# Kernel optimization log

Measured on AMD Instinct MI355X. Metric: run time of the kernel, lower is better.

Reference implementation:

```python
import jax, jax.numpy as jnp
import numpy as np

# C2fBoT config (matches init_kwargs)
B, C1, C2, N, F, HEADS, E = 8, 512, 512, 2, 32, 4, 0.5
C = int(C2 * E)          # hidden channels = 256
HD = C // HEADS          # head_dim = 64
BN_EPS = 1e-3            # ultralytics Conv uses BatchNorm2d(eps=0.001)


def conv2d(x, w, pad):
    # x: [B,Cin,H,W], w: [Cout,Cin,kh,kw]
    return jax.lax.conv_general_dilated(
        x, w, (1, 1), [(pad, pad), (pad, pad)],
        dimension_numbers=("NCHW", "OIHW", "NCHW"))


def bn_eval(x, p):
    # p: [4,C] rows = gamma, beta, running_mean, running_var (inference BN)
    g, b, m, v = p
    s = (g / jnp.sqrt(v + BN_EPS))[:, None, None]
    return (x - m[:, None, None]) * s + b[:, None, None]


def cbs(x, w, p, pad):
    # YOLO Conv block: Conv2d -> BN -> SiLU
    return jax.nn.silu(bn_eval(conv2d(x, w, pad), p))


def bot_attention(x, qkv_w, rw, rh):
    # x: [B,C,H,W]; 1x1-conv QKV + learned relative position bias
    b, c, h, w = x.shape
    hw = h * w
    qkv = conv2d(x, qkv_w, 0).reshape(b, 3, HEADS, HD, hw)
    q, k, v = qkv[:, 0], qkv[:, 1], qkv[:, 2]           # [B,heads,hd,HW]
    r = (rw + rh).reshape(1, HEADS, HD, hw)              # rel-pos content
    # q^T@k*scale + q^T@r*scale == q^T@(k+r)*scale (r broadcasts over batch)
    logits = jnp.einsum('bhdi,bhdj->bhij', q, k + r) * (HD ** -0.5)
    a = jax.nn.softmax(logits, axis=-1)                  # [B,heads,HW,HW]
    out = jnp.einsum('bhij,bhdj->bhdi', a, v)            # [B,heads,hd,HW]
    return out.reshape(b, c, h, w)


def setup_inputs() -> dict:
    key = jax.random.key(0)
    ks = iter(jax.random.split(key, 32))
    def nrm(shape, s=0.05):
        return jax.random.normal(next(ks), shape, jnp.float32) * s
    def bnp(cc):
        return jnp.stack([
            1.0 + 0.1 * jax.random.normal(next(ks), (cc,), jnp.float32),  # gamma
            0.1 * jax.random.normal(next(ks), (cc,), jnp.float32),        # beta
            0.1 * jax.random.normal(next(ks), (cc,), jnp.float32),        # mean
            0.5 + jax.random.uniform(next(ks), (cc,), jnp.float32),       # var
        ])
    return {
        "x": jax.random.normal(next(ks), (B, C1, F, F), jnp.float32),
        "cv1_w": nrm((2 * C, C1, 1, 1)),
        "cv1_bn": bnp(2 * C),
        "cv2_w": nrm((C2, (2 + N) * C, 1, 1)),
        "cv2_bn": bnp(C2),
        "m_cv1_w": nrm((N, C, C, 3, 3)),
        "m_cv1_bn": jnp.stack([bnp(C) for _ in range(N)]),
        "m_qkv_w": nrm((N, 3 * C, C, 1, 1)),
        "m_rw": jax.random.normal(next(ks), (N, 1, HEADS, HD, 1, F), jnp.float32),
        "m_rh": jax.random.normal(next(ks), (N, 1, HEADS, HD, F, 1), jnp.float32),
        "m_cv2_w": nrm((N, C, C, 1, 1)),
        "m_cv2_bn": jnp.stack([bnp(C) for _ in range(N)]),
    }


def reference(x, cv1_w, cv1_bn, cv2_w, cv2_bn,
              m_cv1_w, m_cv1_bn, m_qkv_w, m_rw, m_rh, m_cv2_w, m_cv2_bn):
    t = cbs(x, cv1_w, cv1_bn, 0)                 # [B,2C,H,W]
    ys = [t[:, :C], t[:, C:]]                    # chunk(2, dim=1)
    for i in range(N):                           # fixed small layer loop
        yi = ys[-1]
        z = cbs(yi, m_cv1_w[i], m_cv1_bn[i], 1)  # 3x3 Conv-BN-SiLU
        z = bot_attention(z, m_qkv_w[i], m_rw[i], m_rh[i])
        z = jax.nn.silu(bn_eval(conv2d(z, m_cv2_w[i], 0), m_cv2_bn[i]))
        ys.append(yi + z)                        # shortcut (c1 == c2)
    return cbs(jnp.concatenate(ys, axis=1), cv2_w, cv2_bn, 0)
```

## Files before the change

kernel.cpp:

```cpp
#include <hip/hip_runtime.h>
#include <hip/hip_bf16.h>

typedef unsigned short ushort_t;
typedef __bf16 bf16x8 __attribute__((ext_vector_type(8)));
typedef float f32x4 __attribute__((ext_vector_type(4)));
typedef unsigned short us8 __attribute__((ext_vector_type(8)));
typedef unsigned short us4 __attribute__((ext_vector_type(4)));

#define AS1 __attribute__((address_space(1)))
#define AS3 __attribute__((address_space(3)))

#if __has_builtin(__builtin_amdgcn_exp2f)
#define EXP2F __builtin_amdgcn_exp2f
#else
#define EXP2F exp2f
#endif

__device__ __forceinline__ void gld16(const void* g, void* l){
  __builtin_amdgcn_global_load_lds((AS1 void*)(void*)g, (AS3 void*)l, 16, 0, 0);
}
__device__ __forceinline__ f32x4 mfma16(bf16x8 a, bf16x8 b, f32x4 c){
  return __builtin_amdgcn_mfma_f32_16x16x32_bf16(a, b, c, 0, 0, 0);
}
__device__ __forceinline__ unsigned short f2bfu(float f){
  union { float f; unsigned int i; } c; c.f = f;
  unsigned int x = c.i;
  return (unsigned short)((x + 0x7fffu + ((x >> 16) & 1u)) >> 16);
}
__device__ __forceinline__ float bfu2f(unsigned short u){
  union { unsigned int i; float f; } c; c.i = ((unsigned int)u) << 16; return c.f;
}
__device__ __forceinline__ float dsilu(float x){ return x / (1.f + __expf(-x)); }

__global__ __launch_bounds__(256)
void transpose_x_k(const float* __restrict__ x, ushort_t* __restrict__ xc)
{
  __shared__ float tl[64*68];
  const int ci0 = blockIdx.x*64, px0 = blockIdx.y*64, b = blockIdx.z;
  const int t = threadIdx.x;
  {
    const int ci_l = t>>2, pc = (t&3)*16;
    const float* src = x + (size_t)b*524288 + (size_t)(ci0+ci_l)*1024 + px0 + pc;
    float* d = &tl[ci_l*68 + pc];
    *(float4*)(d)    = *(const float4*)(src);
    *(float4*)(d+4)  = *(const float4*)(src+4);
    *(float4*)(d+8)  = *(const float4*)(src+8);
    *(float4*)(d+12) = *(const float4*)(src+12);
  }
  __syncthreads();
  {
    const int px_l = t>>2, cc = (t&3)*16;
    us8 o0, o1;
#pragma unroll
    for (int i = 0; i < 8; i++) o0[i] = f2bfu(tl[(cc+i)*68 + px_l]);
#pragma unroll
    for (int i = 0; i < 8; i++) o1[i] = f2bfu(tl[(cc+8+i)*68 + px_l]);
    ushort_t* dst = xc + (size_t)b*524288 + (size_t)(px0+px_l)*512 + ci0 + cc;
    *(us8*)dst = o0; *(us8*)(dst+8) = o1;
  }
}

__global__ __launch_bounds__(256)
void cvt4_k(const float* s0, const float* s1, const float* s2, const float* s3,
            ushort_t* d0, ushort_t* d1, ushort_t* d2, ushort_t* d3,
            int n0, int n1, int n2, int n3)
{
  const int seg = blockIdx.y;
  const float* s = (seg==0?s0:seg==1?s1:seg==2?s2:s3);
  ushort_t* d    = (seg==0?d0:seg==1?d1:seg==2?d2:d3);
  const int n4   = (seg==0?n0:seg==1?n1:seg==2?n2:n3) >> 2;
  for (int i = blockIdx.x*256 + threadIdx.x; i < n4; i += gridDim.x*256){
    const float4 v = *(const float4*)(s + (size_t)i*4);
    ushort4 p; p.x=f2bfu(v.x); p.y=f2bfu(v.y); p.z=f2bfu(v.z); p.w=f2bfu(v.w);
    *(ushort4*)(d + (size_t)i*4) = p;
  }
}

__global__ __launch_bounds__(256)
void reorder3_k(const float* __restrict__ w, ushort_t* __restrict__ o,
                ushort_t* __restrict__ zb)
{
  const int blk = blockIdx.x;
  if (blk == 0 && threadIdx.x < 64) zb[threadIdx.x] = 0;
  const float* src = w + (size_t)blk*2304;
  ushort_t* dst = o + (size_t)blk*2304;
  for (int idx = threadIdx.x; idx < 2304; idx += 256){
    const int ci = idx/9, tap = idx - ci*9;
    dst[tap*256 + ci] = f2bfu(src[idx]);
  }
}

template<int BMODE, int EPI, int NT>
__global__ __launch_bounds__(256, 4)
void gemm_k(const ushort_t* __restrict__ A, const int M, const int K, const int kplen,
            const ushort_t* __restrict__ B0, const ushort_t* __restrict__ B1,
            const ushort_t* __restrict__ B2, const ushort_t* __restrict__ B3,
            const int Rb, const long Bbs,
            const float* __restrict__ bnp,
            const float* __restrict__ rw, const float* __restrict__ rh,
            const ushort_t* __restrict__ res, const long res_bs, const int res_rs,
            ushort_t* __restrict__ vtout, const ushort_t* __restrict__ zb,
            void* __restrict__ outp, const long out_bs, const int out_rs)
{
  constexpr int NW = NT/4;
  constexpr int NF = NW/16;
  constexpr int CH = 8 + NT/8;
  constexpr int CPW = CH/4;
  const int m0 = blockIdx.x*64, n0 = blockIdx.y*NT;
  const int bz = blockIdx.z, b = bz & 7, part = bz >> 3;
  const int tid = threadIdx.x, lane = tid & 63, w = tid >> 6;
  const int q = lane >> 4, l15 = lane & 15;
  const int crow8 = lane >> 3, kq8 = lane & 7;
  const int gq8 = kq8 ^ crow8;
  const int r7 = l15 & 7;
  __shared__ __align__(16) ushort_t A_s[64*64];
  __shared__ __align__(16) ushort_t B_s[NT*64];

  f32x4 acc[4][NF];
#pragma unroll
  for (int mi = 0; mi < 4; mi++)
#pragma unroll
    for (int ni = 0; ni < NF; ni++) acc[mi][ni] = (f32x4){0.f,0.f,0.f,0.f};

  const int kbeg = part*kplen, kend_ = kbeg + kplen;
  for (int k0 = kbeg; k0 < kend_; k0 += 64){
    const int kk = k0 + gq8*8;
#pragma unroll
    for (int p = 0; p < CPW; p++){
      const int c = w*CPW + p;
      if (c < 8){
        const int row = c*8 + crow8;
        gld16(A + (size_t)(m0 + row)*K + kk, A_s + c*512);
      } else {
        const int cb = c - 8;
        const int row = cb*8 + crow8;
        const ushort_t* gb;
        if (BMODE == 0){
          gb = B0 + (size_t)b*Bbs + (size_t)(n0 + row)*Rb + kk;
        } else if (BMODE == 1){
          const int seg = kk >> 8;
          const ushort_t* sb = (seg==0?B0:seg==1?B1:seg==2?B2:B3);
          const int sstr = (seg < 2) ? 512 : 256;
          const long sbs = (seg < 2) ? 524288L : 262144L;
          gb = sb + (size_t)b*sbs + (size_t)(n0 + row)*sstr + (kk & 255);
        } else {
          const int tap = k0 >> 8;
          const int ci = (k0 & 255) + gq8*8;
          const int oy = tap/3 - 1, ox = tap - (tap/3)*3 - 1;
          const int px = n0 + row;
          const int yy = (px >> 5) + oy, xx = (px & 31) + ox;
          const bool vld = ((unsigned)yy < 32u) && ((unsigned)xx < 32u);
          gb = vld ? (B0 + (size_t)b*Bbs + (size_t)(yy*32 + xx)*Rb + ci) : zb;
        }
        gld16(gb, B_s + cb*512);
      }
    }
    __syncthreads();
#pragma unroll
    for (int ks = 0; ks < 2; ks++){
      const int slot = (ks*4 + q) ^ r7;
      bf16x8 af[4], bfr[NF];
#pragma unroll
      for (int mi = 0; mi < 4; mi++)
        af[mi] = __builtin_bit_cast(bf16x8, *(const us8*)&A_s[(mi*16 + l15)*64 + slot*8]);
#pragma unroll
      for (int ni = 0; ni < NF; ni++)
        bfr[ni] = __builtin_bit_cast(bf16x8, *(const us8*)&B_s[(w*NW + ni*16 + l15)*64 + slot*8]);
#pragma unroll
      for (int mi = 0; mi < 4; mi++)
#pragma unroll
        for (int ni = 0; ni < NF; ni++)
          acc[mi][ni] = mfma16(af[mi], bfr[ni], acc[mi][ni]);
    }
    __syncthreads();
  }

  const int n_w = n0 + w*NW;
#pragma unroll
  for (int mi = 0; mi < 4; mi++){
    const int mb = m0 + mi*16 + q*4;
    float sc[4], off[4];
    if (EPI != 1 && EPI != 4){
      const float4 g  = *(const float4*)(bnp + mb);
      const float4 be = *(const float4*)(bnp + M + mb);
      const float4 mu = *(const float4*)(bnp + 2*M + mb);
      const float4 va = *(const float4*)(bnp + 3*M + mb);
      sc[0] = g.x/sqrtf(va.x+1e-3f); off[0] = be.x - mu.x*sc[0];
      sc[1] = g.y/sqrtf(va.y+1e-3f); off[1] = be.y - mu.y*sc[1];
      sc[2] = g.z/sqrtf(va.z+1e-3f); off[2] = be.z - mu.z*sc[2];
      sc[3] = g.w/sqrtf(va.w+1e-3f); off[3] = be.w - mu.w*sc[3];
    }
    const int region = mb >> 8;
#pragma unroll
    for (int ni = 0; ni < NF; ni++){
      const int n_g = n_w + ni*16 + l15;
      f32x4 v = acc[mi][ni];
      if (EPI == 4){
        *(float4*)((float*)outp + ((size_t)(part*8 + b)*1024 + n_g)*256 + mb) =
            (float4){v[0], v[1], v[2], v[3]};
        continue;
      }
      float o[4];
#pragma unroll
      for (int r = 0; r < 4; r++){
        float xv = v[r];
        if (EPI == 1){
          if (region == 0) xv *= 0.18033688011112042f;
          else if (region == 1){
            const int c64 = mb + r - 256;
            xv += rw[c64*32 + (n_g & 31)] + rh[c64*32 + (n_g >> 5)];
          }
        } else {
          xv = dsilu(xv*sc[r] + off[r]);
          if (EPI == 2)
            xv += bfu2f(res[(size_t)b*res_bs + (size_t)n_g*res_rs + mb + r]);
        }
        o[r] = xv;
      }
      if (EPI == 3){
        float* of = (float*)outp + (size_t)b*out_bs;
#pragma unroll
        for (int r = 0; r < 4; r++) of[(size_t)(mb + r)*1024 + n_g] = o[r];
      } else if (EPI == 1 && region == 2){
#pragma unroll
        for (int r = 0; r < 4; r++)
          vtout[(size_t)b*262144 + (size_t)(mb + r - 512)*1024 + n_g] = f2bfu(o[r]);
      } else {
        ushort4 pk; pk.x=f2bfu(o[0]); pk.y=f2bfu(o[1]); pk.z=f2bfu(o[2]); pk.w=f2bfu(o[3]);
        *(ushort4*)((ushort_t*)outp + (size_t)b*out_bs + (size_t)n_g*out_rs + mb) = pk;
      }
    }
  }
}

__global__ __launch_bounds__(256)
void reduce3_k(const float* __restrict__ pbuf, const float* __restrict__ bnp,
               ushort_t* __restrict__ out)
{
  const int idx = blockIdx.x*256 + threadIdx.x;
  const int co = (idx & 63)*4;
  const size_t e = (size_t)idx*4;
  float4 a = *(const float4*)(pbuf + e);
  const float4 c = *(const float4*)(pbuf + 2097152 + e);
  a.x += c.x; a.y += c.y; a.z += c.z; a.w += c.w;
  const float4 g  = *(const float4*)(bnp + co);
  const float4 be = *(const float4*)(bnp + 256 + co);
  const float4 mu = *(const float4*)(bnp + 512 + co);
  const float4 va = *(const float4*)(bnp + 768 + co);
  float s0 = g.x/sqrtf(va.x+1e-3f), s1 = g.y/sqrtf(va.y+1e-3f);
  float s2 = g.z/sqrtf(va.z+1e-3f), s3 = g.w/sqrtf(va.w+1e-3f);
  ushort4 pk;
  pk.x = f2bfu(dsilu((a.x - mu.x)*s0 + be.x));
  pk.y = f2bfu(dsilu((a.y - mu.y)*s1 + be.y));
  pk.z = f2bfu(dsilu((a.z - mu.z)*s2 + be.z));
  pk.w = f2bfu(dsilu((a.w - mu.w)*s3 + be.w));
  *(ushort4*)(out + e) = pk;
}

__global__ __launch_bounds__(256)
void attn_k(const ushort_t* __restrict__ qk, const ushort_t* __restrict__ vt,
            ushort_t* __restrict__ out)
{
  const int it = blockIdx.x, h = blockIdx.y, b = blockIdx.z;
  const int tid = threadIdx.x, lane = tid & 63, w = tid >> 6;
  const int q = lane >> 4, l15 = lane & 15;
  const int i0 = it*64;
  __shared__ __align__(16) ushort_t K_s[2][4096];
  __shared__ __align__(16) ushort_t V_s[2][4096];
  __shared__ __align__(16) ushort_t P_s[4096];

  const ushort_t* qkb = qk + (size_t)b*524288;
  const ushort_t* vtb = vt + (size_t)b*262144 + (size_t)h*1024*64;

  const int srow = lane >> 3;
  const int sgq  = (lane & 7) ^ srow;
  const int rs7  = l15 & 7;

  bf16x8 qf[2];
  {
    const ushort_t* qr = qkb + (size_t)(i0 + w*16 + l15)*512 + h*64 + q*8;
    qf[0] = __builtin_bit_cast(bf16x8, *(const us8*)qr);
    qf[1] = __builtin_bit_cast(bf16x8, *(const us8*)(qr + 32));
  }
  f32x4 oacc[4];
#pragma unroll
  for (int nd = 0; nd < 4; nd++) oacc[nd] = (f32x4){0.f,0.f,0.f,0.f};
  float m_s = -3e38f, l_s = 0.f;

#define STAGE(JT, BUF) {                                                        \
    const int j0s = (JT)*64;                                                    \
    _Pragma("unroll")                                                           \
    for (int p = 0; p < 2; p++){                                                \
      const int c = w*2 + p;                                                    \
      const int row = c*8 + srow;                                               \
      gld16(qkb + (size_t)(j0s + row)*512 + 256 + h*64 + sgq*8, &K_s[BUF][c*512]); \
      gld16(vtb + (size_t)row*1024 + j0s + sgq*8, &V_s[BUF][c*512]);            \
    }                                                                           \
  }

  STAGE(0, 0);
  int cur = 0;
  for (int jt = 0; jt < 16; jt++){
    __syncthreads();
    if (jt < 15){ STAGE(jt+1, cur^1); }
    f32x4 sacc[4];
#pragma unroll
    for (int ni = 0; ni < 4; ni++) sacc[ni] = (f32x4){0.f,0.f,0.f,0.f};
#pragma unroll
    for (int ks = 0; ks < 2; ks++){
      const int slot = (ks*4 + q) ^ rs7;
#pragma unroll
      for (int ni = 0; ni < 4; ni++){
        const bf16x8 kf = __builtin_bit_cast(bf16x8,
            *(const us8*)&K_s[cur][(ni*16 + l15)*64 + slot*8]);
        sacc[ni] = mfma16(kf, qf[ks], sacc[ni]);
      }
    }
    float mx = sacc[0][0];
#pragma unroll
    for (int ni = 0; ni < 4; ni++)
#pragma unroll
      for (int r = 0; r < 4; r++) mx = fmaxf(mx, sacc[ni][r]);
    mx = fmaxf(mx, __shfl_xor(mx, 16));
    mx = fmaxf(mx, __shfl_xor(mx, 32));
    const float mnew = fmaxf(m_s, mx);
    const float alpha = EXP2F(m_s - mnew);
    m_s = mnew;
    float p[4][4];
    float ps = 0.f;
#pragma unroll
    for (int ni = 0; ni < 4; ni++)
#pragma unroll
      for (int r = 0; r < 4; r++){ p[ni][r] = EXP2F(sacc[ni][r] - mnew); ps += p[ni][r]; }
    ps += __shfl_xor(ps, 16);
    ps += __shfl_xor(ps, 32);
    l_s = l_s*alpha + ps;
#pragma unroll
    for (int r = 0; r < 4; r++){
      const float a_r = __shfl(alpha, q*4 + r);
#pragma unroll
      for (int nd = 0; nd < 4; nd++) oacc[nd][r] *= a_r;
    }
    {
      const int prow = w*16 + l15;
#pragma unroll
      for (int ni = 0; ni < 4; ni++){
        const int qtr = ni*2 + (q>>1);
        us4 pk = { f2bfu(p[ni][0]), f2bfu(p[ni][1]), f2bfu(p[ni][2]), f2bfu(p[ni][3]) };
        *(us4*)&P_s[prow*64 + ((qtr ^ rs7)<<3) + ((q&1)<<2)] = pk;
      }
    }
#pragma unroll
    for (int ks = 0; ks < 2; ks++){
      const int slot = (ks*4 + q) ^ rs7;
      const bf16x8 pa = __builtin_bit_cast(bf16x8,
          *(const us8*)&P_s[(w*16 + l15)*64 + slot*8]);
#pragma unroll
      for (int nd = 0; nd < 4; nd++){
        const bf16x8 vb = __builtin_bit_cast(bf16x8,
            *(const us8*)&V_s[cur][(nd*16 + l15)*64 + slot*8]);
        oacc[nd] = mfma16(pa, vb, oacc[nd]);
      }
    }
    cur ^= 1;
  }
#undef STAGE
  ushort_t* ob = out + (size_t)b*262144;
#pragma unroll
  for (int r = 0; r < 4; r++){
    const float rinv = 1.f / __shfl(l_s, q*4 + r);
    const size_t rowo = (size_t)(i0 + w*16 + q*4 + r)*256 + h*64 + l15;
#pragma unroll
    for (int nd = 0; nd < 4; nd++)
      ob[rowo + nd*16] = f2bfu(oacc[nd][r]*rinv);
  }
}

extern "C" void kernel_launch(void* const* d_in, const int* in_sizes, int n_in,
                              void* d_out, int out_size, void* d_ws, size_t ws_size,
                              hipStream_t stream)
{
  const float* x       = (const float*)d_in[0];
  const float* cv1_w   = (const float*)d_in[1];
  const float* cv1_bn  = (const float*)d_in[2];
  const float* cv2_w   = (const float*)d_in[3];
  const float* cv2_bn  = (const float*)d_in[4];
  const float* mcv1_w  = (const float*)d_in[5];
  const float* mcv1_bn = (const float*)d_in[6];
  const float* mqkv_w  = (const float*)d_in[7];
  const float* mrw     = (const float*)d_in[8];
  const float* mrh     = (const float*)d_in[9];
  const float* mcv2_w  = (const float*)d_in[10];
  const float* mcv2_bn = (const float*)d_in[11];

  ushort_t* uw = (ushort_t*)d_ws;
  ushort_t* x_cl    = uw;
  ushort_t* t_cl    = x_cl    + 4194304;
  ushort_t* wb_cv1  = t_cl    + 4194304;
  ushort_t* wb_cv2  = wb_cv1  + 262144;
  ushort_t* wb_qkv  = wb_cv2  + 524288;
  ushort_t* wb_mcv2 = wb_qkv  + 393216;
  ushort_t* wb_mcv1 = wb_mcv2 + 131072;
  ushort_t* z1_cl   = wb_mcv1 + 1179648;
  ushort_t* qk_cl   = z1_cl   + 2097152;
  ushort_t* vt_b    = qk_cl   + 4194304;
  ushort_t* att_cl  = vt_b    + 2097152;
  ushort_t* y2_cl   = att_cl  + 2097152;
  ushort_t* y3_cl   = y2_cl   + 2097152;
  float*    part_f  = (float*)(y3_cl + 2097152);
  ushort_t* zbuf    = (ushort_t*)(part_f + 4194304);

  const dim3 blk(256);

  transpose_x_k<<<dim3(8,16,8), blk, 0, stream>>>(x, x_cl);
  cvt4_k<<<dim3(256,4), blk, 0, stream>>>(cv1_w, cv2_w, mqkv_w, mcv2_w,
                                          wb_cv1, wb_cv2, wb_qkv, wb_mcv2,
                                          262144, 524288, 393216, 131072);
  reorder3_k<<<dim3(512), blk, 0, stream>>>(mcv1_w, wb_mcv1, zbuf);

  gemm_k<0,0,128><<<dim3(8,8,8), blk, 0, stream>>>(
      wb_cv1, 512, 512, 512, x_cl, nullptr, nullptr, nullptr, 512, 524288L,
      cv1_bn, nullptr, nullptr, nullptr, 0, 0, nullptr, nullptr, t_cl, 524288L, 512);

  const ushort_t* yi = t_cl + 256;  long yi_bs = 524288; int yi_rs = 512;
  ushort_t* youts[2] = { y2_cl, y3_cl };
  for (int i = 0; i < 2; i++){
    gemm_k<2,4,128><<<dim3(4,8,16), blk, 0, stream>>>(
        wb_mcv1 + (size_t)i*589824, 256, 2304, 1152, yi, nullptr, nullptr, nullptr,
        yi_rs, yi_bs,
        nullptr, nullptr, nullptr, nullptr, 0, 0, nullptr, zbuf, part_f, 0, 0);
    reduce3_k<<<dim3(2048), blk, 0, stream>>>(part_f, mcv1_bn + i*1024, z1_cl);
    gemm_k<0,1,128><<<dim3(12,8,8), blk, 0, stream>>>(
        wb_qkv + (size_t)i*196608, 768, 256, 256, z1_cl, nullptr, nullptr, nullptr, 256, 262144L,
        nullptr, mrw + i*8192, mrh + i*8192, nullptr, 0, 0, vt_b, nullptr, qk_cl, 524288L, 512);
    attn_k<<<dim3(16,4,8), blk, 0, stream>>>(qk_cl, vt_b, att_cl);
    gemm_k<0,2,64><<<dim3(4,16,8), blk, 0, stream>>>(
        wb_mcv2 + (size_t)i*65536, 256, 256, 256, att_cl, nullptr, nullptr, nullptr, 256, 262144L,
        mcv2_bn + i*1024, nullptr, nullptr, yi, yi_bs, yi_rs, nullptr, nullptr,
        youts[i], 262144L, 256);
    yi = youts[i]; yi_bs = 262144; yi_rs = 256;
  }

  gemm_k<1,3,128><<<dim3(8,8,8), blk, 0, stream>>>(
      wb_cv2, 512, 1024, 1024, t_cl, t_cl + 256, y2_cl, y3_cl, 0, 0,
      cv2_bn, nullptr, nullptr, nullptr, 0, 0, nullptr, nullptr, (float*)d_out, 524288L, 0);
}
```

Measured before the change: 304.3 us.

## Merge prep kernels into one launch and widen attention key tiles to 128

Folds the input transpose, the weight conversions and the 3x3 weight reorder into a single prep kernel, so two kernel launches disappear. The attention kernel now processes 128 keys per tile instead of 64, which halves the loop trip count and the barriers, and uses new XOR swizzles for V and P in shared memory. P is packed to bf16 by truncation with a byte-perm instead of round-to-nearest. The trade-offs are more shared memory and registers per block, which may lower occupancy, and slightly different rounding of P.

```diff
diff --git a/kernel.cpp b/kernel.cpp
--- a/kernel.cpp
+++ b/kernel.cpp
@@ -5,7 +5,7 @@
 typedef __bf16 bf16x8 __attribute__((ext_vector_type(8)));
 typedef float f32x4 __attribute__((ext_vector_type(4)));
 typedef unsigned short us8 __attribute__((ext_vector_type(8)));
-typedef unsigned short us4 __attribute__((ext_vector_type(4)));
+typedef unsigned int u32;
 
 #define AS1 __attribute__((address_space(1)))
 #define AS3 __attribute__((address_space(3)))
@@ -31,62 +31,68 @@
   union { unsigned int i; float f; } c; c.i = ((unsigned int)u) << 16; return c.f;
 }
 __device__ __forceinline__ float dsilu(float x){ return x / (1.f + __expf(-x)); }
+__device__ __forceinline__ u32 pack_trunc(float a, float b){
+  union { float f; u32 u; } ca, cb; ca.f = a; cb.f = b;
+#if __has_builtin(__builtin_amdgcn_perm)
+  return __builtin_amdgcn_perm(cb.u, ca.u, 0x07060302u);
+#else
+  return (cb.u & 0xFFFF0000u) | (ca.u >> 16);
+#endif
+}
 
 __global__ __launch_bounds__(256)
-void transpose_x_k(const float* __restrict__ x, ushort_t* __restrict__ xc)
+void prep_k(const float* __restrict__ x, ushort_t* __restrict__ xc,
+            const float* __restrict__ s0, const float* __restrict__ s1,
+            const float* __restrict__ s2, const float* __restrict__ s3,
+            ushort_t* __restrict__ d0, ushort_t* __restrict__ d1,
+            ushort_t* __restrict__ d2, ushort_t* __restrict__ d3,
+            const float* __restrict__ w3, ushort_t* __restrict__ o3,
+            ushort_t* __restrict__ zb)
 {
   __shared__ float tl[64*68];
-  const int ci0 = blockIdx.x*64, px0 = blockIdx.y*64, b = blockIdx.z;
-  const int t = threadIdx.x;
-  {
-    const int ci_l = t>>2, pc = (t&3)*16;
-    const float* src = x + (size_t)b*524288 + (size_t)(ci0+ci_l)*1024 + px0 + pc;
-    float* d = &tl[ci_l*68 + pc];
-    *(float4*)(d)    = *(const float4*)(src);
-    *(float4*)(d+4)  = *(const float4*)(src+4);
-    *(float4*)(d+8)  = *(const float4*)(src+8);
-    *(float4*)(d+12) = *(const float4*)(src+12);
-  }
-  __syncthreads();
-  {
-    const int px_l = t>>2, cc = (t&3)*16;
-    us8 o0, o1;
-#pragma unroll
-    for (int i = 0; i < 8; i++) o0[i] = f2bfu(tl[(cc+i)*68 + px_l]);
-#pragma unroll
-    for (int i = 0; i < 8; i++) o1[i] = f2bfu(tl[(cc+8+i)*68 + px_l]);
-    ushort_t* dst = xc + (size_t)b*524288 + (size_t)(px0+px_l)*512 + ci0 + cc;
-    *(us8*)dst = o0; *(us8*)(dst+8) = o1;
-  }
-}
-
-__global__ __launch_bounds__(256)
-void cvt4_k(const float* s0, const float* s1, const float* s2, const float* s3,
-            ushort_t* d0, ushort_t* d1, ushort_t* d2, ushort_t* d3,
-            int n0, int n1, int n2, int n3)
-{
-  const int seg = blockIdx.y;
-  const float* s = (seg==0?s0:seg==1?s1:seg==2?s2:s3);
-  ushort_t* d    = (seg==0?d0:seg==1?d1:seg==2?d2:d3);
-  const int n4   = (seg==0?n0:seg==1?n1:seg==2?n2:n3) >> 2;
-  for (int i = blockIdx.x*256 + threadIdx.x; i < n4; i += gridDim.x*256){
-    const float4 v = *(const float4*)(s + (size_t)i*4);
-    ushort4 p; p.x=f2bfu(v.x); p.y=f2bfu(v.y); p.z=f2bfu(v.z); p.w=f2bfu(v.w);
-    *(ushort4*)(d + (size_t)i*4) = p;
-  }
-}
-
-__global__ __launch_bounds__(256)
-void reorder3_k(const float* __restrict__ w, ushort_t* __restrict__ o,
-                ushort_t* __restrict__ zb)
-{
-  const int blk = blockIdx.x;
-  if (blk == 0 && threadIdx.x < 64) zb[threadIdx.x] = 0;
-  const float* src = w + (size_t)blk*2304;
-  ushort_t* dst = o + (size_t)blk*2304;
-  for (int idx = threadIdx.x; idx < 2304; idx += 256){
-    const int ci = idx/9, tap = idx - ci*9;
-    dst[tap*256 + ci] = f2bfu(src[idx]);
+  const int bx = blockIdx.x, t = threadIdx.x;
+  if (bx < 1024){
+    const int b = bx >> 7, ci0 = (bx & 7)*64, px0 = ((bx >> 3) & 15)*64;
+    {
+      const int ci_l = t>>2, pc = (t&3)*16;
+      const float* src = x + (size_t)b*524288 + (size_t)(ci0+ci_l)*1024 + px0 + pc;
+      float* d = &tl[ci_l*68 + pc];
+      *(float4*)(d)    = *(const float4*)(src);
+      *(float4*)(d+4)  = *(const float4*)(src+4);
+      *(float4*)(d+8)  = *(const float4*)(src+8);
+      *(float4*)(d+12) = *(const float4*)(src+12);
+    }
+    __syncthreads();
+    {
+      const int px_l = t>>2, cc = (t&3)*16;
+      us8 o0, o1;
+#pragma unroll
+      for (int i = 0; i < 8; i++) o0[i] = f2bfu(tl[(cc+i)*68 + px_l]);
+#pragma unroll
+      for (int i = 0; i < 8; i++) o1[i] = f2bfu(tl[(cc+8+i)*68 + px_l]);
+      ushort_t* dst = xc + (size_t)b*524288 + (size_t)(px0+px_l)*512 + ci0 + cc;
+      *(us8*)dst = o0; *(us8*)(dst+8) = o1;
+    }
+  } else if (bx < 2048){
+    const int bb = bx - 1024;
+    const int seg = bb >> 8, blk = bb & 255;
+    const float* s = (seg==0?s0:seg==1?s1:seg==2?s2:s3);
+    ushort_t* d    = (seg==0?d0:seg==1?d1:seg==2?d2:d3);
+    const int n4   = (seg==0?262144:seg==1?524288:seg==2?393216:131072) >> 2;
+    for (int i = blk*256 + t; i < n4; i += 256*256){
+      const float4 v = *(const float4*)(s + (size_t)i*4);
+      ushort4 p; p.x=f2bfu(v.x); p.y=f2bfu(v.y); p.z=f2bfu(v.z); p.w=f2bfu(v.w);
+      *(ushort4*)(d + (size_t)i*4) = p;
+    }
+  } else {
+    const int blk = bx - 2048;
+    if (blk == 0 && t < 64) zb[t] = 0;
+    const float* src = w3 + (size_t)blk*2304;
+    ushort_t* dst = o3 + (size_t)blk*2304;
+    for (int idx = t; idx < 2304; idx += 256){
+      const int ci = idx/9, tap = idx - ci*9;
+      dst[tap*256 + ci] = f2bfu(src[idx]);
+    }
   }
 }
 
@@ -265,16 +271,18 @@
   const int tid = threadIdx.x, lane = tid & 63, w = tid >> 6;
   const int q = lane >> 4, l15 = lane & 15;
   const int i0 = it*64;
-  __shared__ __align__(16) ushort_t K_s[2][4096];
-  __shared__ __align__(16) ushort_t V_s[2][4096];
-  __shared__ __align__(16) ushort_t P_s[4096];
+  __shared__ __align__(16) ushort_t K_s[2][8192];
+  __shared__ __align__(16) ushort_t V_s[2][8192];
+  __shared__ __align__(16) ushort_t P_s[8192];
 
   const ushort_t* qkb = qk + (size_t)b*524288;
-  const ushort_t* vtb = vt + (size_t)b*262144 + (size_t)h*1024*64;
-
-  const int srow = lane >> 3;
-  const int sgq  = (lane & 7) ^ srow;
-  const int rs7  = l15 & 7;
+  const ushort_t* vtb = vt + (size_t)b*262144 + (size_t)h*65536;
+
+  const int k_row8 = lane >> 3;
+  const int k_gq   = (lane & 7) ^ k_row8;
+  const int v_row4 = lane >> 4;
+  const int v_s16  = lane & 15;
+  const int rs7    = l15 & 7;
 
   bf16x8 qf[2];
   {
@@ -288,29 +296,31 @@
   float m_s = -3e38f, l_s = 0.f;
 
 #define STAGE(JT, BUF) {                                                        \
-    const int j0s = (JT)*64;                                                    \
+    const int j0s = (JT)*128;                                                   \
     _Pragma("unroll")                                                           \
-    for (int p = 0; p < 2; p++){                                                \
-      const int c = w*2 + p;                                                    \
-      const int row = c*8 + srow;                                               \
-      gld16(qkb + (size_t)(j0s + row)*512 + 256 + h*64 + sgq*8, &K_s[BUF][c*512]); \
-      gld16(vtb + (size_t)row*1024 + j0s + sgq*8, &V_s[BUF][c*512]);            \
+    for (int p = 0; p < 4; p++){                                                \
+      const int c = w*4 + p;                                                    \
+      const int krow = c*8 + k_row8;                                            \
+      gld16(qkb + (size_t)(j0s + krow)*512 + 256 + h*64 + k_gq*8, &K_s[BUF][c*512]); \
+      const int vrow = c*4 + v_row4;                                            \
+      const int vg = v_s16 ^ (vrow & 15);                                       \
+      gld16(vtb + (size_t)vrow*1024 + j0s + vg*8, &V_s[BUF][c*512]);            \
     }                                                                           \
   }
 
   STAGE(0, 0);
   int cur = 0;
-  for (int jt = 0; jt < 16; jt++){
+  for (int jt = 0; jt < 8; jt++){
     __syncthreads();
-    if (jt < 15){ STAGE(jt+1, cur^1); }
-    f32x4 sacc[4];
-#pragma unroll
-    for (int ni = 0; ni < 4; ni++) sacc[ni] = (f32x4){0.f,0.f,0.f,0.f};
+    if (jt < 7){ STAGE(jt+1, cur^1); }
+    f32x4 sacc[8];
+#pragma unroll
+    for (int ni = 0; ni < 8; ni++) sacc[ni] = (f32x4){0.f,0.f,0.f,0.f};
 #pragma unroll
     for (int ks = 0; ks < 2; ks++){
       const int slot = (ks*4 + q) ^ rs7;
 #pragma unroll
-      for (int ni = 0; ni < 4; ni++){
+      for (int ni = 0; ni < 8; ni++){
         const bf16x8 kf = __builtin_bit_cast(bf16x8,
             *(const us8*)&K_s[cur][(ni*16 + l15)*64 + slot*8]);
         sacc[ni] = mfma16(kf, qf[ks], sacc[ni]);
@@ -318,7 +328,7 @@
     }
     float mx = sacc[0][0];
 #pragma unroll
-    for (int ni = 0; ni < 4; ni++)
+    for (int ni = 0; ni < 8; ni++)
 #pragma unroll
       for (int r = 0; r < 4; r++) mx = fmaxf(mx, sacc[ni][r]);
     mx = fmaxf(mx, __shfl_xor(mx, 16));
@@ -326,10 +336,10 @@
     const float mnew = fmaxf(m_s, mx);
     const float alpha = EXP2F(m_s - mnew);
     m_s = mnew;
-    float p[4][4];
+    float p[8][4];
     float ps = 0.f;
 #pragma unroll
-    for (int ni = 0; ni < 4; ni++)
+    for (int ni = 0; ni < 8; ni++)
 #pragma unroll
       for (int r = 0; r < 4; r++){ p[ni][r] = EXP2F(sacc[ni][r] - mnew); ps += p[ni][r]; }
     ps += __shfl_xor(ps, 16);
@@ -344,21 +354,23 @@
     {
       const int prow = w*16 + l15;
 #pragma unroll
-      for (int ni = 0; ni < 4; ni++){
-        const int qtr = ni*2 + (q>>1);
-        us4 pk = { f2bfu(p[ni][0]), f2bfu(p[ni][1]), f2bfu(p[ni][2]), f2bfu(p[ni][3]) };
-        *(us4*)&P_s[prow*64 + ((qtr ^ rs7)<<3) + ((q&1)<<2)] = pk;
-      }
-    }
-#pragma unroll
-    for (int ks = 0; ks < 2; ks++){
-      const int slot = (ks*4 + q) ^ rs7;
+      for (int ni = 0; ni < 8; ni++){
+        uint2 pk;
+        pk.x = pack_trunc(p[ni][0], p[ni][1]);
+        pk.y = pack_trunc(p[ni][2], p[ni][3]);
+        const int phys = (ni*2 + (q>>1)) ^ l15;
+        *(uint2*)&P_s[prow*128 + phys*8 + (q&1)*4] = pk;
+      }
+    }
+#pragma unroll
+    for (int ks = 0; ks < 4; ks++){
+      const int slotp = (ks*4 + q) ^ l15;
       const bf16x8 pa = __builtin_bit_cast(bf16x8,
-          *(const us8*)&P_s[(w*16 + l15)*64 + slot*8]);
+          *(const us8*)&P_s[(w*16 + l15)*128 + slotp*8]);
 #pragma unroll
       for (int nd = 0; nd < 4; nd++){
         const bf16x8 vb = __builtin_bit_cast(bf16x8,
-            *(const us8*)&V_s[cur][(nd*16 + l15)*64 + slot*8]);
+            *(const us8*)&V_s[cur][(nd*16 + l15)*128 + slotp*8]);
         oacc[nd] = mfma16(pa, vb, oacc[nd]);
       }
     }
@@ -412,11 +424,9 @@
 
   const dim3 blk(256);
 
-  transpose_x_k<<<dim3(8,16,8), blk, 0, stream>>>(x, x_cl);
-  cvt4_k<<<dim3(256,4), blk, 0, stream>>>(cv1_w, cv2_w, mqkv_w, mcv2_w,
-                                          wb_cv1, wb_cv2, wb_qkv, wb_mcv2,
-                                          262144, 524288, 393216, 131072);
-  reorder3_k<<<dim3(512), blk, 0, stream>>>(mcv1_w, wb_mcv1, zbuf);
+  prep_k<<<dim3(2560), blk, 0, stream>>>(x, x_cl,
+      cv1_w, cv2_w, mqkv_w, mcv2_w, wb_cv1, wb_cv2, wb_qkv, wb_mcv2,
+      mcv1_w, wb_mcv1, zbuf);
 
   gemm_k<0,0,128><<<dim3(8,8,8), blk, 0, stream>>>(
       wb_cv1, 512, 512, 512, x_cl, nullptr, nullptr, nullptr, 512, 524288L,
```

New measurement: 295.3 us. 1.03x faster.
